# Optimization experiments

Measured on AMD Instinct MI355X. Metric: run time of the kernel, lower is better.

The kernel has to match this reference:

```python
import jax, jax.numpy as jnp
import numpy as np

B, L, D, H = 2, 2048, 1024, 16
DK = D // H  # 64


def setup_inputs() -> dict:
    key = jax.random.key(0)
    ks = jax.random.split(key, 9)
    s = 0.02
    return {
        "x": jax.random.normal(ks[0], (B, L, D), dtype=jnp.float32),
        "wq": jax.random.normal(ks[1], (D, D), dtype=jnp.float32) * s,
        "bq": jax.random.normal(ks[2], (D,), dtype=jnp.float32) * s,
        "wk": jax.random.normal(ks[3], (D, D), dtype=jnp.float32) * s,
        "bk": jax.random.normal(ks[4], (D,), dtype=jnp.float32) * s,
        "wv": jax.random.normal(ks[5], (D, D), dtype=jnp.float32) * s,
        "bv": jax.random.normal(ks[6], (D,), dtype=jnp.float32) * s,
        "wo": jax.random.normal(ks[7], (D, D), dtype=jnp.float32) * s,
        "bo": jax.random.normal(ks[8], (D,), dtype=jnp.float32) * s,
    }


def reference(x, wq, bq, wk, bk, wv, bv, wo, bo):
    b, l, d = x.shape
    # torch nn.Linear: y = x @ W^T + b
    q = (x @ wq.T + bq).reshape(b, l, H, DK).transpose(0, 2, 1, 3)  # (b,h,l,dk)
    k = (x @ wk.T + bk).reshape(b, l, H, DK).transpose(0, 2, 1, 3)
    v = (x @ wv.T + bv).reshape(b, l, H, DK).transpose(0, 2, 1, 3)
    scale = 1.0 / jnp.sqrt(jnp.asarray(DK, dtype=x.dtype))
    scores = jnp.einsum("bhqd,bhkd->bhqk", q, k) * scale  # (b,h,l,l)
    causal = jnp.triu(jnp.ones((l, l), dtype=bool), k=1)  # True above diagonal -> masked
    scores = jnp.where(causal[None, None], -jnp.inf, scores)
    probs = jax.nn.softmax(scores, axis=-1)
    out = jnp.einsum("bhqk,bhkd->bhqd", probs, v)  # (b,h,l,dk)
    out = out.transpose(0, 2, 1, 3).reshape(b, l, d)
    return out @ wo.T + bo
```

## Files before the change

kernel.cpp:

```cpp
#include <hip/hip_runtime.h>
#include <cstdint>

#define SEQ     2048
#define DMODEL  1024
#define NHEAD   16
#define DKH     64
#define NTOK    4096
#define LDQKV   3072

typedef __bf16 bf16x8 __attribute__((ext_vector_type(8)));
typedef __bf16 bf16x4 __attribute__((ext_vector_type(4)));
typedef float  f32x4  __attribute__((ext_vector_type(4)));

#define MFMA_BF16(a, b, c) __builtin_amdgcn_mfma_f32_16x16x32_bf16((a), (b), (c), 0, 0, 0)

#define C2F 0.18033688f

__device__ inline float fast_exp2(float x) {
#if __has_builtin(__builtin_amdgcn_exp2f)
  return __builtin_amdgcn_exp2f(x);
#else
  return __expf(x * 0.69314718056f);
#endif
}

__device__ inline void async_copy16(const void* g, void* l) {
  __builtin_amdgcn_global_load_lds(
      reinterpret_cast<const __attribute__((address_space(1))) void*>(
          reinterpret_cast<uintptr_t>(g)),
      reinterpret_cast<__attribute__((address_space(3))) void*>(
          reinterpret_cast<uintptr_t>(l)),
      16, 0, 0);
}

__device__ inline bf16x4 cvt4(float4 v) {
  bf16x4 r;
  r[0] = (__bf16)v.x; r[1] = (__bf16)v.y; r[2] = (__bf16)v.z; r[3] = (__bf16)v.w;
  return r;
}

__global__ __launch_bounds__(256) void pack_kernel(
    const float4* __restrict__ x,
    const float4* __restrict__ wq, const float4* __restrict__ wk,
    const float4* __restrict__ wv, const float4* __restrict__ wo,
    const float4* __restrict__ bq, const float4* __restrict__ bk,
    const float4* __restrict__ bv,
    bf16x4* __restrict__ xb, bf16x4* __restrict__ wqkv,
    bf16x4* __restrict__ wob, float4* __restrict__ bcat)
{
  const int NX = NTOK * DMODEL / 4;
  const int NW = DMODEL * DMODEL / 4;
  const int TOT = NX + 4 * NW + 3 * (DMODEL / 4);
  for (int g = blockIdx.x * 256 + threadIdx.x; g < TOT; g += gridDim.x * 256) {
    if (g < NX) {
      xb[g] = cvt4(x[g]);
    } else if (g < NX + 3 * NW) {
      int g2 = g - NX;
      const float4* s = (g2 < NW) ? wq : (g2 < 2 * NW ? wk : wv);
      float4 v = s[g2 & (NW - 1)];
      if (g2 < NW) { v.x *= C2F; v.y *= C2F; v.z *= C2F; v.w *= C2F; }
      wqkv[g2] = cvt4(v);
    } else if (g < NX + 4 * NW) {
      int g3 = g - NX - 3 * NW;
      wob[g3] = cvt4(wo[g3]);
    } else {
      int g4 = g - NX - 4 * NW;
      const float4* s = (g4 < 256) ? bq : (g4 < 512 ? bk : bv);
      float4 v = s[g4 & 255];
      if (g4 < 256) { v.x *= C2F; v.y *= C2F; v.z *= C2F; v.w *= C2F; }
      bcat[g4] = v;
    }
  }
}

template<int BN>
__global__ __launch_bounds__(256) void gemm_bias(
    const __bf16* __restrict__ A, const __bf16* __restrict__ W,
    const float* __restrict__ bias, void* __restrict__ C,
    int ldc, int out_bf16)
{
  constexpr int K = 1024;
  constexpr int JT = BN / 32;
  __shared__ __bf16 sA[2][128 * 32];
  __shared__ __bf16 sB[2][BN * 32];
  const int tid  = threadIdx.x;
  const int wave = tid >> 6, lane = tid & 63;
  const int quad = lane >> 4, l16 = lane & 15;
  const size_t m0 = (size_t)blockIdx.x * 128;
  const size_t n0 = (size_t)blockIdx.y * BN;
  const int wm = (wave & 1) * 64, wn = (wave >> 1) * (BN / 2);

  const int g0 = wave * 2;
  const int sr = lane >> 2;
  const int sc = (lane & 3) * 8;
  const __bf16* pa0 = A + (m0 + g0 * 16 + sr) * K + sc;
  const __bf16* pa1 = pa0 + 16 * K;
  const int brow = (BN == 128) ? g0 * 16 : wave * 16;
  const __bf16* pb0 = W + (n0 + brow + sr) * K + sc;
  const int lo  = g0 * 512;
  const int lob = (BN == 128) ? g0 * 512 : wave * 512;

  f32x4 acc[4][JT];
  const f32x4 z = {0.f, 0.f, 0.f, 0.f};
#pragma unroll
  for (int i = 0; i < 4; ++i)
#pragma unroll
    for (int j = 0; j < JT; ++j) acc[i][j] = z;

  async_copy16(pa0, &sA[0][lo]);
  async_copy16(pa1, &sA[0][lo + 512]);
  async_copy16(pb0, &sB[0][lob]);
  if (BN == 128) async_copy16(pb0 + 16 * K, &sB[0][lob + 512]);

  for (int k0 = 0; k0 < K; k0 += 32) {
    const int cur = (k0 >> 5) & 1, nxt = cur ^ 1;
    __syncthreads();
    if (k0 + 32 < K) {
      async_copy16(pa0 + k0 + 32, &sA[nxt][lo]);
      async_copy16(pa1 + k0 + 32, &sA[nxt][lo + 512]);
      async_copy16(pb0 + k0 + 32, &sB[nxt][lob]);
      if (BN == 128) async_copy16(pb0 + 16 * K + k0 + 32, &sB[nxt][lob + 512]);
    }

    bf16x8 af[4], bw[JT];
#pragma unroll
    for (int i = 0; i < 4; ++i)
      af[i] = *(const bf16x8*)(&sA[cur][(wm + i * 16 + l16) * 32 + quad * 8]);
#pragma unroll
    for (int j = 0; j < JT; ++j)
      bw[j] = *(const bf16x8*)(&sB[cur][(wn + j * 16 + l16) * 32 + quad * 8]);
#pragma unroll
    for (int i = 0; i < 4; ++i)
#pragma unroll
      for (int j = 0; j < JT; ++j)
        acc[i][j] = MFMA_BF16(af[i], bw[j], acc[i][j]);
  }

  float bi[JT];
#pragma unroll
  for (int j = 0; j < JT; ++j) bi[j] = bias[n0 + wn + j * 16 + l16];

#pragma unroll
  for (int i = 0; i < 4; ++i) {
#pragma unroll
    for (int j = 0; j < JT; ++j) {
#pragma unroll
      for (int r = 0; r < 4; ++r) {
        size_t row = m0 + wm + i * 16 + quad * 4 + r;
        size_t col = n0 + wn + j * 16 + l16;
        float v = acc[i][j][r] + bi[j];
        if (out_bf16) ((__bf16*)C)[row * ldc + col] = (__bf16)v;
        else          ((float*)C)[row * ldc + col] = v;
      }
    }
  }
}

__global__ __launch_bounds__(256) void vtrans_kernel(
    const __bf16* __restrict__ qkv, __bf16* __restrict__ vt)
{
  __shared__ __bf16 t[64][66];
  const int tid = threadIdx.x;
  const int bh = blockIdx.x;
  const int b = bh >> 4, h = bh & 15;
  const int l0 = blockIdx.y * 64;
  const int r4 = tid >> 6;
  const int c  = tid & 63;
#pragma unroll
  for (int rep = 0; rep < 16; ++rep) {
    int ll = rep * 4 + r4;
    t[ll][c] = qkv[(size_t)(b * SEQ + l0 + ll) * LDQKV + 2048 + h * DKH + c];
  }
  __syncthreads();
#pragma unroll
  for (int rep = 0; rep < 16; ++rep) {
    int dk = rep * 4 + r4;
    vt[(size_t)(bh * DKH + dk) * SEQ + l0 + c] = t[c][dk];
  }
}

__global__ __launch_bounds__(256) void attn_kernel(
    const __bf16* __restrict__ qkv,
    const __bf16* __restrict__ vt,
    __bf16* __restrict__ attn)
{
  __shared__ __bf16 sK[2][64 * 64];
  __shared__ __bf16 sV[2][64 * 64];
  __shared__ __bf16 pbuf[4][2][16 * 64];
  const int tid  = threadIdx.x;
  const int wave = tid >> 6, lane = tid & 63;
  const int quad = lane >> 4, l16 = lane & 15;
  const int id = blockIdx.x;
  const int u = (id >> 3) & 15, v = id & 7, w = id >> 7;
  const int bh = v * 4 + w;
  const int ue = u ^ ((w >> 1) * 15);
  const int qb = (w & 1) ? ue : 15 - ue;
  const int b = bh >> 4, h = bh & 15;
  const int q0 = qb * 128;
  const int qw = q0 + wave * 32;
  const size_t tokbase = (size_t)b * SEQ;

  const int srow = lane >> 3;
  const int sgr  = (lane & 7) ^ srow;
  const __bf16* pKsrc = qkv + (tokbase + wave * 16 + srow) * LDQKV + 1024 + h * DKH + sgr * 8;
  const __bf16* pVsrc = vt + ((size_t)bh * DKH + wave * 16 + srow) * SEQ + sgr * 8;
  const int lo = wave * 16 * 64;

  bf16x8 qf[2][2];
#pragma unroll
  for (int hf = 0; hf < 2; ++hf)
#pragma unroll
    for (int s = 0; s < 2; ++s)
      qf[hf][s] = *(const bf16x8*)(qkv + (tokbase + qw + hf * 16 + l16) * LDQKV
                                   + h * DKH + s * 32 + quad * 8);

  bf16x8 ones;
#pragma unroll
  for (int i = 0; i < 8; ++i) ones[i] = (__bf16)1.0f;

  f32x4 o[2][4], lacc[2];
  const f32x4 z = {0.f, 0.f, 0.f, 0.f};
#pragma unroll
  for (int hf = 0; hf < 2; ++hf) {
#pragma unroll
    for (int t = 0; t < 4; ++t) o[hf][t] = z;
    lacc[hf] = z;
  }

  const int swl = l16 & 7;
  const int ntiles = 2 * qb + 2;

  async_copy16(pKsrc, &sK[0][lo]);
  async_copy16(pKsrc + (size_t)8 * LDQKV, &sK[0][lo + 8 * 64]);
  async_copy16(pVsrc, &sV[0][lo]);
  async_copy16(pVsrc + (size_t)8 * SEQ, &sV[0][lo + 8 * 64]);

  for (int t0 = 0; t0 < ntiles; ++t0) {
    const int cur = t0 & 1, nxt = cur ^ 1;
    const int key0 = t0 * 64;
    __syncthreads();
    if (t0 + 1 < ntiles) {
      const size_t koff = (size_t)(t0 + 1) * 64;
      async_copy16(pKsrc + koff * LDQKV, &sK[nxt][lo]);
      async_copy16(pKsrc + (koff + 8) * LDQKV, &sK[nxt][lo + 8 * 64]);
      async_copy16(pVsrc + koff, &sV[nxt][lo]);
      async_copy16(pVsrc + (size_t)8 * SEQ + koff, &sV[nxt][lo + 8 * 64]);
    }
    const __bf16* K_ = &sK[cur][0];
    const __bf16* V_ = &sV[cur][0];

    f32x4 sacc[2][4];
#pragma unroll
    for (int ct = 0; ct < 4; ++ct) {
      bf16x8 k0 = *(const bf16x8*)(K_ + (ct * 16 + l16) * 64 + ((quad ^ swl) * 8));
      bf16x8 k1 = *(const bf16x8*)(K_ + (ct * 16 + l16) * 64 + (((4 + quad) ^ swl) * 8));
#pragma unroll
      for (int hf = 0; hf < 2; ++hf) {
        sacc[hf][ct] = MFMA_BF16(k0, qf[hf][0], z);
        sacc[hf][ct] = MFMA_BF16(k1, qf[hf][1], sacc[hf][ct]);
      }
    }

    const bool fullv = (key0 + 63 <= qw);
#pragma unroll
    for (int hf = 0; hf < 2; ++hf) {
      __bf16* pb = &pbuf[wave][hf][0];
#pragma unroll
      for (int ct = 0; ct < 4; ++ct) {
        bf16x4 p4;
        if (fullv) {
#pragma unroll
          for (int r = 0; r < 4; ++r) p4[r] = (__bf16)fast_exp2(sacc[hf][ct][r]);
        } else {
#pragma unroll
          for (int r = 0; r < 4; ++r) {
            float sv = (key0 + ct * 16 + quad * 4 + r <= qw + hf * 16 + l16)
                           ? sacc[hf][ct][r] : -1e30f;
            p4[r] = (__bf16)fast_exp2(sv);
          }
        }
        *(bf16x4*)(pb + l16 * 64 + (((ct * 4 + quad) ^ (swl << 1)) * 4)) = p4;
      }
    }

    bf16x8 ap[2][2];
#pragma unroll
    for (int hf = 0; hf < 2; ++hf) {
      const __bf16* pb = &pbuf[wave][hf][0];
      ap[hf][0] = *(const bf16x8*)(pb + l16 * 64 + ((quad ^ swl) * 8));
      ap[hf][1] = *(const bf16x8*)(pb + l16 * 64 + (((4 + quad) ^ swl) * 8));
      lacc[hf] = MFMA_BF16(ap[hf][0], ones, lacc[hf]);
      lacc[hf] = MFMA_BF16(ap[hf][1], ones, lacc[hf]);
    }
#pragma unroll
    for (int dt = 0; dt < 4; ++dt) {
      bf16x8 v0 = *(const bf16x8*)(V_ + (dt * 16 + l16) * 64 + ((quad ^ swl) * 8));
      bf16x8 v1 = *(const bf16x8*)(V_ + (dt * 16 + l16) * 64 + (((4 + quad) ^ swl) * 8));
#pragma unroll
      for (int hf = 0; hf < 2; ++hf) {
        o[hf][dt] = MFMA_BF16(ap[hf][0], v0, o[hf][dt]);
        o[hf][dt] = MFMA_BF16(ap[hf][1], v1, o[hf][dt]);
      }
    }
  }

#pragma unroll
  for (int hf = 0; hf < 2; ++hf) {
    float linv[4];
#pragma unroll
    for (int r = 0; r < 4; ++r) linv[r] = 1.0f / lacc[hf][r];
#pragma unroll
    for (int dt = 0; dt < 4; ++dt)
#pragma unroll
      for (int r = 0; r < 4; ++r)
        attn[(tokbase + qw + hf * 16 + quad * 4 + r) * DMODEL + h * DKH + dt * 16 + l16] =
            (__bf16)(o[hf][dt][r] * linv[r]);
  }
}

extern "C" void kernel_launch(void* const* d_in, const int* in_sizes, int n_in,
                              void* d_out, int out_size, void* d_ws, size_t ws_size,
                              hipStream_t stream) {
  const float* x  = (const float*)d_in[0];
  const float* wq = (const float*)d_in[1];
  const float* bq = (const float*)d_in[2];
  const float* wk = (const float*)d_in[3];
  const float* bk = (const float*)d_in[4];
  const float* wv = (const float*)d_in[5];
  const float* bv = (const float*)d_in[6];
  const float* wo = (const float*)d_in[7];
  const float* bo = (const float*)d_in[8];

  char* ws = (char*)d_ws;
  __bf16* xb    = (__bf16*)(ws + 0);
  __bf16* wqkv  = (__bf16*)(ws + 8388608);
  __bf16* wob   = (__bf16*)(ws + 14680064);
  float*  bcat  = (float*)(ws + 16777216);
  __bf16* qkv   = (__bf16*)(ws + 16789504);
  __bf16* vt    = (__bf16*)(ws + 41955328);
  __bf16* attn  = (__bf16*)(ws + 50343936);
  float*  out   = (float*)d_out;

  pack_kernel<<<1024, 256, 0, stream>>>(
      (const float4*)x, (const float4*)wq, (const float4*)wk, (const float4*)wv,
      (const float4*)wo, (const float4*)bq, (const float4*)bk, (const float4*)bv,
      (bf16x4*)xb, (bf16x4*)wqkv, (bf16x4*)wob, (float4*)bcat);

  gemm_bias<128><<<dim3(32, 24), 256, 0, stream>>>(xb, wqkv, bcat, qkv, LDQKV, 1);

  vtrans_kernel<<<dim3(32, 32), 256, 0, stream>>>(qkv, vt);

  attn_kernel<<<512, 256, 0, stream>>>(qkv, vt, attn);

  gemm_bias<64><<<dim3(32, 16), 256, 0, stream>>>(attn, wob, bo, out, DMODEL, 0);
}
```

Baseline: 185.5 us.

## Split attention into single-wave blocks of 32 query rows each

The attention kernel now runs as 2048 single-wave blocks, each owning 32 query rows, in place of 512 four-wave blocks covering 128 rows. Each block skips key tiles beyond its own causal limit and loads its full K/V tile with one wave, and the block-to-work mapping is rotated to spread causal load across the grid. The aim is finer causal work skipping and better load balance. In exchange, K/V tiles are no longer shared across four waves, so L2/global traffic into LDS rises about fourfold.

After: 216.1 us. 1.16x slower.

```diff
diff --git a/kernel.cpp b/kernel.cpp
--- a/kernel.cpp
+++ b/kernel.cpp
@@ -179,32 +179,28 @@
   }
 }
 
-__global__ __launch_bounds__(256) void attn_kernel(
+__global__ __launch_bounds__(64) void attn_kernel(
     const __bf16* __restrict__ qkv,
     const __bf16* __restrict__ vt,
     __bf16* __restrict__ attn)
 {
   __shared__ __bf16 sK[2][64 * 64];
   __shared__ __bf16 sV[2][64 * 64];
-  __shared__ __bf16 pbuf[4][2][16 * 64];
-  const int tid  = threadIdx.x;
-  const int wave = tid >> 6, lane = tid & 63;
+  __shared__ __bf16 pbuf[2][16 * 64];
+  const int lane = threadIdx.x & 63;
   const int quad = lane >> 4, l16 = lane & 15;
   const int id = blockIdx.x;
-  const int u = (id >> 3) & 15, v = id & 7, w = id >> 7;
-  const int bh = v * 4 + w;
-  const int ue = u ^ ((w >> 1) * 15);
-  const int qb = (w & 1) ? ue : 15 - ue;
+  const int v = id & 7, u = (id >> 3) & 63, t = (id >> 9) & 3;
+  const int bh = v * 4 + t;
+  const int qb = ((63 - u) + t * 16) & 63;
   const int b = bh >> 4, h = bh & 15;
-  const int q0 = qb * 128;
-  const int qw = q0 + wave * 32;
+  const int qw = qb * 32;
   const size_t tokbase = (size_t)b * SEQ;
 
   const int srow = lane >> 3;
   const int sgr  = (lane & 7) ^ srow;
-  const __bf16* pKsrc = qkv + (tokbase + wave * 16 + srow) * LDQKV + 1024 + h * DKH + sgr * 8;
-  const __bf16* pVsrc = vt + ((size_t)bh * DKH + wave * 16 + srow) * SEQ + sgr * 8;
-  const int lo = wave * 16 * 64;
+  const __bf16* pKsrc = qkv + (tokbase + srow) * LDQKV + 1024 + h * DKH + sgr * 8;
+  const __bf16* pVsrc = vt + ((size_t)bh * DKH + srow) * SEQ + sgr * 8;
 
   bf16x8 qf[2][2];
 #pragma unroll
@@ -223,17 +219,18 @@
 #pragma unroll
   for (int hf = 0; hf < 2; ++hf) {
 #pragma unroll
-    for (int t = 0; t < 4; ++t) o[hf][t] = z;
+    for (int tt = 0; tt < 4; ++tt) o[hf][tt] = z;
     lacc[hf] = z;
   }
 
   const int swl = l16 & 7;
-  const int ntiles = 2 * qb + 2;
-
-  async_copy16(pKsrc, &sK[0][lo]);
-  async_copy16(pKsrc + (size_t)8 * LDQKV, &sK[0][lo + 8 * 64]);
-  async_copy16(pVsrc, &sV[0][lo]);
-  async_copy16(pVsrc + (size_t)8 * SEQ, &sV[0][lo + 8 * 64]);
+  const int ntiles = (qb >> 1) + 1;
+
+#pragma unroll
+  for (int c = 0; c < 8; ++c) {
+    async_copy16(pKsrc + (size_t)(c * 8) * LDQKV, &sK[0][c * 512]);
+    async_copy16(pVsrc + (size_t)(c * 8) * SEQ, &sV[0][c * 512]);
+  }
 
   for (int t0 = 0; t0 < ntiles; ++t0) {
     const int cur = t0 & 1, nxt = cur ^ 1;
@@ -241,10 +238,11 @@
     __syncthreads();
     if (t0 + 1 < ntiles) {
       const size_t koff = (size_t)(t0 + 1) * 64;
-      async_copy16(pKsrc + koff * LDQKV, &sK[nxt][lo]);
-      async_copy16(pKsrc + (koff + 8) * LDQKV, &sK[nxt][lo + 8 * 64]);
-      async_copy16(pVsrc + koff, &sV[nxt][lo]);
-      async_copy16(pVsrc + (size_t)8 * SEQ + koff, &sV[nxt][lo + 8 * 64]);
+#pragma unroll
+      for (int c = 0; c < 8; ++c) {
+        async_copy16(pKsrc + (koff + c * 8) * LDQKV, &sK[nxt][c * 512]);
+        async_copy16(pVsrc + koff + (size_t)(c * 8) * SEQ, &sV[nxt][c * 512]);
+      }
     }
     const __bf16* K_ = &sK[cur][0];
     const __bf16* V_ = &sV[cur][0];
@@ -264,7 +262,7 @@
     const bool fullv = (key0 + 63 <= qw);
 #pragma unroll
     for (int hf = 0; hf < 2; ++hf) {
-      __bf16* pb = &pbuf[wave][hf][0];
+      __bf16* pb = &pbuf[hf][0];
 #pragma unroll
       for (int ct = 0; ct < 4; ++ct) {
         bf16x4 p4;
@@ -286,7 +284,7 @@
     bf16x8 ap[2][2];
 #pragma unroll
     for (int hf = 0; hf < 2; ++hf) {
-      const __bf16* pb = &pbuf[wave][hf][0];
+      const __bf16* pb = &pbuf[hf][0];
       ap[hf][0] = *(const bf16x8*)(pb + l16 * 64 + ((quad ^ swl) * 8));
       ap[hf][1] = *(const bf16x8*)(pb + l16 * 64 + (((4 + quad) ^ swl) * 8));
       lacc[hf] = MFMA_BF16(ap[hf][0], ones, lacc[hf]);
@@ -350,7 +348,7 @@
 
   vtrans_kernel<<<dim3(32, 32), 256, 0, stream>>>(qkv, vt);
 
-  attn_kernel<<<512, 256, 0, stream>>>(qkv, vt, attn);
+  attn_kernel<<<2048, 64, 0, stream>>>(qkv, vt, attn);
 
   gemm_bias<64><<<dim3(32, 16), 256, 0, stream>>>(attn, wob, bo, out, DMODEL, 0);
 }
```
